# Performance work log

Measured on AMD Instinct MI355X. Metric: run time of the kernel, lower is better.

Reference implementation:

```python
import jax, jax.numpy as jnp
import numpy as np

B, N, DIM, H, DH, M = 4, 1024, 1024, 16, 64, 16  # batch, seq, model dim, heads, head dim, num_mem_kv
QK_SCALE = 10.0  # qk_norm_scale


def l2norm(t, eps=1e-12):
    # F.normalize(t, dim=-1) with clamp_min(eps), groups=1
    n = jnp.linalg.norm(t, axis=-1, keepdims=True)
    return t / jnp.maximum(n, eps)


def rotate_half(x):
    # interleaved pairs: (x0,x1) -> (-x1, x0)
    x = x.reshape(*x.shape[:-1], -1, 2)
    x1, x2 = x[..., 0], x[..., 1]
    return jnp.stack((-x2, x1), axis=-1).reshape(*x.shape[:-2], x.shape[-2] * 2)


def apply_rope(t, freqs):
    # freqs: [n, d], t: [b, h, n, d]
    return t * jnp.cos(freqs) + rotate_half(t) * jnp.sin(freqs)


def setup_inputs() -> dict:
    key = jax.random.key(0)
    ks = jax.random.split(key, 14)
    x = jax.random.normal(ks[0], (B, N, DIM), dtype=jnp.float32)
    # rotary freqs: outer(pos, inv_freq) with each freq repeated twice (interleaved pairs)
    pos = jnp.arange(N, dtype=jnp.float32)
    inv_freq = 1.0 / (10000.0 ** (jnp.arange(0, DH, 2, dtype=jnp.float32) / DH))
    freqs = jnp.repeat(pos[:, None] * inv_freq[None, :], 2, axis=-1)  # [N, DH]
    s = 0.02
    Wq = jax.random.normal(ks[1], (DIM, H * DH), dtype=jnp.float32) * s
    Wk = jax.random.normal(ks[2], (DIM, H * DH), dtype=jnp.float32) * s
    Wv = jax.random.normal(ks[3], (DIM, H * DH), dtype=jnp.float32) * s
    q_scale = 1.0 + 0.1 * jax.random.normal(ks[4], (H, 1, DH), dtype=jnp.float32)
    k_scale = 1.0 + 0.1 * jax.random.normal(ks[5], (H, 1, DH), dtype=jnp.float32)
    mem_k = jax.random.normal(ks[6], (H, M, DH), dtype=jnp.float32)
    mem_v = jax.random.normal(ks[7], (H, M, DH), dtype=jnp.float32)
    W_pre = jnp.eye(H, dtype=jnp.float32) + 0.05 * jax.random.normal(ks[8], (H, H), dtype=jnp.float32)
    W_post = jnp.eye(H, dtype=jnp.float32) + 0.05 * jax.random.normal(ks[9], (H, H), dtype=jnp.float32)
    W_hgate = jax.random.normal(ks[10], (DIM, H), dtype=jnp.float32) * s
    b_hgate = jnp.full((H,), 2.0, dtype=jnp.float32)
    W_vgate = jax.random.normal(ks[11], (DIM, H * DH), dtype=jnp.float32) * s
    b_vgate = jnp.full((H * DH,), 2.0, dtype=jnp.float32)
    Wo = jax.random.normal(ks[12], (H * DH, DIM), dtype=jnp.float32) * s
    return dict(x=x, freqs=freqs, Wq=Wq, Wk=Wk, Wv=Wv, q_scale=q_scale, k_scale=k_scale,
                mem_k=mem_k, mem_v=mem_v, W_pre=W_pre, W_post=W_post,
                W_hgate=W_hgate, b_hgate=b_hgate, W_vgate=W_vgate, b_vgate=b_vgate, Wo=Wo)


def reference(x, freqs, Wq, Wk, Wv, q_scale, k_scale, mem_k, mem_v,
              W_pre, W_post, W_hgate, b_hgate, W_vgate, b_vgate, Wo):
    b, n, _ = x.shape
    # projections -> [b, h, n, dh]
    q = (x @ Wq).reshape(b, n, H, DH).transpose(0, 2, 1, 3)
    k = (x @ Wk).reshape(b, n, H, DH).transpose(0, 2, 1, 3)
    v = (x @ Wv).reshape(b, n, H, DH).transpose(0, 2, 1, 3)
    # qk l2-norm (groups=1) + learned per-head dim scales
    q = l2norm(q) * q_scale
    k = l2norm(k) * k_scale
    # rotary (xpos_scale = None -> scale 1)
    q = apply_rope(q, freqs)
    k = apply_rope(k, freqs)
    # memory key/values, prepended along the kv sequence axis
    mk = (l2norm(mem_k) * k_scale)[None].repeat(b, axis=0)  # [b,h,M,dh]
    mv = mem_v[None].repeat(b, axis=0)
    k = jnp.concatenate((mk, k), axis=-2)  # [b,h,M+n,dh]
    v = jnp.concatenate((mv, v), axis=-2)
    i, j = q.shape[-2], k.shape[-2]
    dots = jnp.einsum('bhid,bhjd->bhij', q, k) * QK_SCALE
    dots = jnp.einsum('bhij,gh->bgij', dots, W_pre)  # pre-softmax talking heads
    # causal mask (memory slots at the front are always visible)
    qpos = jnp.arange(i)
    kpos = jnp.arange(j)
    causal = kpos[None, :] > (qpos[:, None] + (j - i))  # True -> masked
    mask_value = -jnp.finfo(dots.dtype).max
    dots = jnp.where(causal[None, None], mask_value, dots)
    attn = jax.nn.softmax(dots, axis=-1)
    attn = jnp.einsum('bhij,gh->bgij', attn, W_post)  # post-softmax talking heads
    out = jnp.einsum('bhij,bhjd->bhid', attn, v)  # [b,h,n,dh]
    # per-head value gate
    head_gate = jax.nn.sigmoid(x @ W_hgate + b_hgate)  # [b,n,h]
    out = out * head_gate.transpose(0, 2, 1)[..., None]
    out = out.transpose(0, 2, 1, 3).reshape(b, n, H * DH)
    # per-dim value gate (sigmoid)
    out = out * jax.nn.sigmoid(x @ W_vgate + b_vgate)
    return out @ Wo
```

## Files before the change

### kernel.cpp

```cpp
#include <hip/hip_runtime.h>
#include <hip/hip_bf16.h>
#include <cmath>

typedef __attribute__((ext_vector_type(8))) short short8;
typedef __attribute__((ext_vector_type(4))) float f32x4;

__device__ __forceinline__ unsigned short to_bf(float f) {
  __hip_bfloat16 h = __float2bfloat16(f);
  return __builtin_bit_cast(unsigned short, h);
}

__global__ __launch_bounds__(256)
void cvt_bf16x4(const float* __restrict__ in, unsigned short* __restrict__ out, int n4)
{
  int i = blockIdx.x * 256 + threadIdx.x;
  if (i < n4) {
    float4 v = ((const float4*)in)[i];
    ushort4 o;
    o.x = to_bf(v.x); o.y = to_bf(v.y); o.z = to_bf(v.z); o.w = to_bf(v.w);
    ((ushort4*)out)[i] = o;
  }
}

__global__ __launch_bounds__(256)
void transpose_to_bf(const float* __restrict__ W, unsigned short* __restrict__ WT)
{
  __shared__ float tile[64][65];
  const int n0 = blockIdx.x * 64, k0 = blockIdx.y * 64;
  const int t = threadIdx.x, c = t & 63, r4 = t >> 6;
#pragma unroll
  for (int q = 0; q < 16; ++q) {
    int r = (q << 2) + r4;
    tile[r][c] = W[(size_t)(k0 + r) * 1024 + n0 + c];
  }
  __syncthreads();
#pragma unroll
  for (int q = 0; q < 16; ++q) {
    int r = (q << 2) + r4;
    WT[(size_t)(n0 + r) * 1024 + k0 + c] = to_bf(tile[c][r]);
  }
}

__global__ __launch_bounds__(256)
void gemm_bf128(const unsigned short* __restrict__ A, const unsigned short* __restrict__ BT,
                float* __restrict__ C, unsigned short* __restrict__ Vout,
                const float* __restrict__ bias2, int mode)
{
  __shared__ __align__(16) unsigned short Ab[128 * 40];
  __shared__ __align__(16) unsigned short Bb[128 * 40];
  const int t = threadIdx.x, lane = t & 63, w = t >> 6;
  const int m = lane & 15, quad = lane >> 4;
  const int wm = w & 1, wn = w >> 1;
  const int row0 = blockIdx.y << 7, col0 = blockIdx.x << 7;

  const int c0 = t,        r0 = c0 >> 2, kp0 = c0 & 3;
  const int c1 = t + 256,  r1 = c1 >> 2, kp1 = c1 & 3;

  f32x4 acc[4][4];
#pragma unroll
  for (int mi = 0; mi < 4; ++mi)
#pragma unroll
    for (int ni = 0; ni < 4; ++ni) acc[mi][ni] = (f32x4){0.f, 0.f, 0.f, 0.f};

  uint4 pa0 = *(const uint4*)(A + (size_t)(row0 + r0) * 1024 + kp0 * 8);
  uint4 pa1 = *(const uint4*)(A + (size_t)(row0 + r1) * 1024 + kp1 * 8);
  uint4 pb0 = *(const uint4*)(BT + (size_t)(col0 + r0) * 1024 + kp0 * 8);
  uint4 pb1 = *(const uint4*)(BT + (size_t)(col0 + r1) * 1024 + kp1 * 8);

  for (int kk = 0; kk < 1024; kk += 32) {
    *(uint4*)((char*)Ab + r0 * 80 + kp0 * 16) = pa0;
    *(uint4*)((char*)Ab + r1 * 80 + kp1 * 16) = pa1;
    *(uint4*)((char*)Bb + r0 * 80 + kp0 * 16) = pb0;
    *(uint4*)((char*)Bb + r1 * 80 + kp1 * 16) = pb1;
    __syncthreads();
    if (kk + 32 < 1024) {
      pa0 = *(const uint4*)(A + (size_t)(row0 + r0) * 1024 + kk + 32 + kp0 * 8);
      pa1 = *(const uint4*)(A + (size_t)(row0 + r1) * 1024 + kk + 32 + kp1 * 8);
      pb0 = *(const uint4*)(BT + (size_t)(col0 + r0) * 1024 + kk + 32 + kp0 * 8);
      pb1 = *(const uint4*)(BT + (size_t)(col0 + r1) * 1024 + kk + 32 + kp1 * 8);
    }
    short8 af[4], bf[4];
#pragma unroll
    for (int mi = 0; mi < 4; ++mi)
      af[mi] = *(const short8*)((char*)Ab + ((wm << 6) + (mi << 4) + m) * 80 + quad * 16);
#pragma unroll
    for (int ni = 0; ni < 4; ++ni)
      bf[ni] = *(const short8*)((char*)Bb + ((wn << 6) + (ni << 4) + m) * 80 + quad * 16);
#pragma unroll
    for (int mi = 0; mi < 4; ++mi)
#pragma unroll
      for (int ni = 0; ni < 4; ++ni)
        acc[mi][ni] = __builtin_amdgcn_mfma_f32_16x16x32_bf16(af[mi], bf[ni], acc[mi][ni], 0, 0, 0);
    __syncthreads();
  }
#pragma unroll
  for (int mi = 0; mi < 4; ++mi)
#pragma unroll
    for (int ni = 0; ni < 4; ++ni)
#pragma unroll
      for (int reg = 0; reg < 4; ++reg) {
        int mrow = row0 + (wm << 6) + (mi << 4) + (quad << 2) + reg;
        int ncol = col0 + (wn << 6) + (ni << 4) + m;
        float v = acc[mi][ni][reg];
        if (mode == 0) {
          C[((size_t)mrow << 10) + ncol] = v;
        } else if (mode == 2) {
          float s = v + bias2[ncol];
          C[((size_t)mrow << 10) + ncol] = 1.f / (1.f + __expf(-s));
        } else {
          int bb = mrow >> 10, nn = mrow & 1023;
          Vout[((size_t)((bb << 10) + ncol)) * 1056 + 16 + nn] = to_bf(v);
        }
      }
}

__global__ __launch_bounds__(256)
void hgate_proj(const float* __restrict__ x, const float* __restrict__ W,
                const float* __restrict__ bias, float* __restrict__ hg)
{
  int G = blockIdx.x * 256 + threadIdx.x;
  int row = G >> 4, h = G & 15;
  const float4* x4 = (const float4*)(x + ((size_t)row << 10));
  float acc = 0.f;
#pragma unroll 4
  for (int k4 = 0; k4 < 256; ++k4) {
    float4 xv = x4[k4];
    int kb = k4 << 2;
    acc += xv.x * W[(kb + 0) * 16 + h] + xv.y * W[(kb + 1) * 16 + h]
         + xv.z * W[(kb + 2) * 16 + h] + xv.w * W[(kb + 3) * 16 + h];
  }
  float v = acc + bias[h];
  hg[(row << 4) + h] = 1.f / (1.f + __expf(-v));
}

__global__ __launch_bounds__(256)
void q_post_bf(const float* __restrict__ q_lin, const float* __restrict__ scale,
               const float* __restrict__ freqs, unsigned short* __restrict__ qb)
{
  int gid = blockIdx.x * 256 + threadIdx.x;
  int d = gid & 63;
  int row = gid >> 6;
  int h = row & 15;
  int n = (row >> 4) & 1023;
  float v = q_lin[gid];
  float ss = v * v;
#pragma unroll
  for (int off = 32; off; off >>= 1) ss += __shfl_xor(ss, off);
  v = v / fmaxf(sqrtf(ss), 1e-12f) * scale[(h << 6) + d];
  float f = freqs[(n << 6) + d];
  float other = __shfl_xor(v, 1);
  float rot = (d & 1) ? other : -other;
  qb[gid] = to_bf((v * cosf(f) + rot * sinf(f)) * 10.f);
}

__global__ __launch_bounds__(256)
void k_post_bf(const float* __restrict__ k_lin, const float* __restrict__ scale,
               const float* __restrict__ freqs, unsigned short* __restrict__ kall)
{
  int gid = blockIdx.x * 256 + threadIdx.x;
  int d = gid & 63;
  int row = gid >> 6;
  int h = row & 15;
  int n = (row >> 4) & 1023;
  int b = row >> 14;
  float v = k_lin[gid];
  float ss = v * v;
#pragma unroll
  for (int off = 32; off; off >>= 1) ss += __shfl_xor(ss, off);
  v = v / fmaxf(sqrtf(ss), 1e-12f) * scale[(h << 6) + d];
  float f = freqs[(n << 6) + d];
  float other = __shfl_xor(v, 1);
  float rot = (d & 1) ? other : -other;
  float out = v * cosf(f) + rot * sinf(f);
  kall[(size_t)(b * 1056 + 16 + n) * 1024 + (h << 6) + d] = to_bf(out);
}

__global__ __launch_bounds__(256)
void mem_build(const float* __restrict__ mem_k, const float* __restrict__ mem_v,
               const float* __restrict__ k_scale,
               unsigned short* __restrict__ kall, unsigned short* __restrict__ vallT)
{
  int gid = blockIdx.x * 256 + threadIdx.x;
  int d = gid & 63;
  int row = gid >> 6;
  int h = row >> 4, mm = row & 15;
  float v = mem_k[gid];
  float ss = v * v;
#pragma unroll
  for (int off = 32; off; off >>= 1) ss += __shfl_xor(ss, off);
  unsigned short kb = to_bf(v / fmaxf(sqrtf(ss), 1e-12f) * k_scale[(h << 6) + d]);
  unsigned short vb = to_bf(mem_v[gid]);
#pragma unroll
  for (int b = 0; b < 4; ++b) {
    kall[(size_t)(b * 1056 + mm) * 1024 + (h << 6) + d] = kb;
    vallT[(size_t)((b << 10) + (h << 6) + d) * 1056 + mm] = vb;
  }
}


__global__ __launch_bounds__(256, 3)
void attn_lsum(const unsigned short* __restrict__ qb, const unsigned short* __restrict__ kall,
               const float* __restrict__ W_pre, float* __restrict__ Lbuf)
{
  __shared__ float sS[16 * 16 * 33];
  __shared__ f32x4 sWpre4[64];

  const int t = threadIdx.x, lane = t & 63, w = t >> 6;
  const int m = lane & 15, quad = lane >> 4;
  if (t < 64) {
    int h = t >> 2, p4 = t & 3;
    sWpre4[t] = (f32x4){W_pre[(4 * p4 + 0) * 16 + h], W_pre[(4 * p4 + 1) * 16 + h],
                        W_pre[(4 * p4 + 2) * 16 + h], W_pre[(4 * p4 + 3) * 16 + h]};
  }

  const int blk = blockIdx.x;
  const int u0 = (4352 * blk) >> 10, u1 = (4352 * (blk + 1)) >> 10;
  if (u0 == u1) return;

  int accu = 0, bi = 0;
  while (true) {
    int un = (((bi & 63) + 1) >> 1) + 1;
    if (accu + un > u0) break;
    accu += un; ++bi;
  }
  int b = bi >> 6, it = bi & 63, uoff = u0 - accu;

  short8 afr[4][2];
  float partL[16];
  bool fresh = true;

  for (int u = u0; u < u1; ++u) {
    const int i0 = it << 4;
    if (fresh) {
#pragma unroll
      for (int hh = 0; hh < 4; ++hh)
#pragma unroll
        for (int kk = 0; kk < 2; ++kk)
          afr[hh][kk] = *(const short8*)(qb + (((size_t)(b << 10) + i0 + m) << 10)
                                         + ((w << 2) + hh) * 64 + kk * 32 + quad * 8);
#pragma unroll
      for (int g = 0; g < 16; ++g) partL[g] = 0.f;
      fresh = false;
    }
    const int j0 = uoff << 5;
#pragma unroll
    for (int sub = 0; sub < 2; ++sub) {
      const int js = j0 + (sub << 4);
#pragma unroll
      for (int hh = 0; hh < 4; ++hh) {
        f32x4 s = (f32x4){0.f, 0.f, 0.f, 0.f};
#pragma unroll
        for (int kk = 0; kk < 2; ++kk) {
          short8 bfr = *(const short8*)(kall + ((size_t)(b * 1056 + js + m) << 10)
                                        + ((w << 2) + hh) * 64 + kk * 32 + quad * 8);
          s = __builtin_amdgcn_mfma_f32_16x16x32_bf16(afr[hh][kk], bfr, s, 0, 0, 0);
        }
#pragma unroll
        for (int reg = 0; reg < 4; ++reg)
          sS[(((w << 2) + hh) * 16 + (quad << 2) + reg) * 33 + (sub << 4) + m] = s[reg];
      }
    }
    __syncthreads();
    {
      const int i_l = t >> 4, j_l = t & 15;
      const int ig = i0 + i_l;
      float ch0[16], ch1[16];
#pragma unroll
      for (int h = 0; h < 16; ++h) {
        ch0[h] = sS[(h * 16 + i_l) * 33 + j_l];
        ch1[h] = sS[(h * 16 + i_l) * 33 + 16 + j_l];
      }
      f32x4 a0[4], a1[4];
#pragma unroll
      for (int p = 0; p < 4; ++p) { a0[p] = (f32x4){0.f,0.f,0.f,0.f}; a1[p] = a0[p]; }
#pragma unroll
      for (int h = 0; h < 16; ++h) {
        float c0 = ch0[h], c1 = ch1[h];
#pragma unroll
        for (int p = 0; p < 4; ++p) {
          f32x4 wv = sWpre4[(h << 2) + p];
          a0[p] += wv * c0;
          a1[p] += wv * c1;
        }
      }
      const bool ok0 = (j0 + j_l) <= ig + 16;
      const bool ok1 = (j0 + 16 + j_l) <= ig + 16;
#pragma unroll
      for (int p = 0; p < 4; ++p)
#pragma unroll
        for (int e = 0; e < 4; ++e) {
          float v0 = ok0 ? __expf(a0[p][e] - 20.f) : 0.f;
          float v1 = ok1 ? __expf(a1[p][e] - 20.f) : 0.f;
          partL[(p << 2) + e] += v0 + v1;
        }
    }
    __syncthreads();
    ++uoff;
    if (uoff == ((it + 1) >> 1) + 1) {
#pragma unroll
      for (int g = 0; g < 16; ++g) {
        float v = partL[g];
        v += __shfl_xor(v, 1); v += __shfl_xor(v, 2);
        v += __shfl_xor(v, 4); v += __shfl_xor(v, 8);
        if (m == 0)
          atomicAdd(&Lbuf[(((size_t)(b << 10) + i0 + (w << 2) + quad) << 4) + g], v);
      }
      ++bi; b = bi >> 6; it = bi & 63; uoff = 0; fresh = true;
    }
  }
  if (!fresh) {
    const int i0 = it << 4;
#pragma unroll
    for (int g = 0; g < 16; ++g) {
      float v = partL[g];
      v += __shfl_xor(v, 1); v += __shfl_xor(v, 2);
      v += __shfl_xor(v, 4); v += __shfl_xor(v, 8);
      if (m == 0)
        atomicAdd(&Lbuf[(((size_t)(b << 10) + i0 + (w << 2) + quad) << 4) + g], v);
    }
  }
}

__global__ __launch_bounds__(256)
void attn_pv2(const unsigned short* __restrict__ qb, const unsigned short* __restrict__ kall,
              const unsigned short* __restrict__ vallT, const float* __restrict__ W_pre,
              const float* __restrict__ W_post, const float* __restrict__ Lbuf,
              float* __restrict__ Obuf)
{
  __shared__ float sS[16 * 16 * 33];
  __shared__ unsigned short sE[16 * 16 * 40];
  __shared__ f32x4 sWpre4[64], sWpost4[64];
  __shared__ float sIL[256];

  const int t = threadIdx.x, lane = t & 63, w = t >> 6;
  const int m = lane & 15, quad = lane >> 4;
  if (t < 64) {
    int h = t >> 2, p4 = t & 3;
    sWpre4[t]  = (f32x4){W_pre[(4 * p4 + 0) * 16 + h],  W_pre[(4 * p4 + 1) * 16 + h],
                         W_pre[(4 * p4 + 2) * 16 + h],  W_pre[(4 * p4 + 3) * 16 + h]};
    sWpost4[t] = (f32x4){W_post[(4 * p4 + 0) * 16 + h], W_post[(4 * p4 + 1) * 16 + h],
                         W_post[(4 * p4 + 2) * 16 + h], W_post[(4 * p4 + 3) * 16 + h]};
  }

  const int blk = blockIdx.x;
  const int u0 = (4352 * blk) >> 9, u1 = (4352 * (blk + 1)) >> 9;
  if (u0 == u1) return;

  int accu = 0, bi = 0;
  while (true) {
    int un = (((bi & 63) + 1) >> 1) + 1;
    if (accu + un > u0) break;
    accu += un; ++bi;
  }
  int b = bi >> 6, it = bi & 63, uoff = u0 - accu;

  short8 afr[4][2];
  f32x4 oacc[4][4];
  bool fresh = true;

  for (int u = u0; u < u1; ++u) {
    const int i0 = it << 4;
    if (fresh) {
#pragma unroll
      for (int hh = 0; hh < 4; ++hh)
#pragma unroll
        for (int kk = 0; kk < 2; ++kk)
          afr[hh][kk] = *(const short8*)(qb + (((size_t)(b << 10) + i0 + m) << 10)
                                         + ((w << 2) + hh) * 64 + kk * 32 + quad * 8);
#pragma unroll
      for (int a = 0; a < 4; ++a)
#pragma unroll
        for (int dt = 0; dt < 4; ++dt) oacc[a][dt] = (f32x4){0.f, 0.f, 0.f, 0.f};
      sIL[t] = 1.f / Lbuf[(((size_t)(b << 10) + i0 + (t >> 4)) << 4) + (t & 15)];
      fresh = false;
    }
    const int j0 = uoff << 5;
#pragma unroll
    for (int sub = 0; sub < 2; ++sub) {
      const int js = j0 + (sub << 4);
#pragma unroll
      for (int hh = 0; hh < 4; ++hh) {
        f32x4 s = (f32x4){0.f, 0.f, 0.f, 0.f};
#pragma unroll
        for (int kk = 0; kk < 2; ++kk) {
          short8 bfr = *(const short8*)(kall + ((size_t)(b * 1056 + js + m) << 10)
                                        + ((w << 2) + hh) * 64 + kk * 32 + quad * 8);
          s = __builtin_amdgcn_mfma_f32_16x16x32_bf16(afr[hh][kk], bfr, s, 0, 0, 0);
        }
#pragma unroll
        for (int reg = 0; reg < 4; ++reg)
          sS[(((w << 2) + hh) * 16 + (quad << 2) + reg) * 33 + (sub << 4) + m] = s[reg];
      }
    }
    __syncthreads();
    {
      const int i_l = t >> 4, j_l = t & 15;
      const int ig = i0 + i_l;
      float ch0[16], ch1[16];
#pragma unroll
      for (int h = 0; h < 16; ++h) {
        ch0[h] = sS[(h * 16 + i_l) * 33 + j_l];
        ch1[h] = sS[(h * 16 + i_l) * 33 + 16 + j_l];
      }
      f32x4 a0[4], a1[4];
#pragma unroll
      for (int p = 0; p < 4; ++p) { a0[p] = (f32x4){0.f,0.f,0.f,0.f}; a1[p] = a0[p]; }
#pragma unroll
      for (int h = 0; h < 16; ++h) {
        float c0 = ch0[h], c1 = ch1[h];
#pragma unroll
        for (int p = 0; p < 4; ++p) {
          f32x4 wv = sWpre4[(h << 2) + p];
          a0[p] += wv * c0;
          a1[p] += wv * c1;
        }
      }
      const bool ok0 = (j0 + j_l) <= ig + 16;
      const bool ok1 = (j0 + 16 + j_l) <= ig + 16;
      float e0[16], e1[16];
#pragma unroll
      for (int p = 0; p < 4; ++p)
#pragma unroll
        for (int e = 0; e < 4; ++e) {
          int g = (p << 2) + e;
          float il = sIL[(i_l << 4) + g];
          e0[g] = ok0 ? __expf(a0[p][e] - 20.f) * il : 0.f;
          e1[g] = ok1 ? __expf(a1[p][e] - 20.f) * il : 0.f;
        }
      f32x4 b0[4], b1[4];
#pragma unroll
      for (int p = 0; p < 4; ++p) { b0[p] = (f32x4){0.f,0.f,0.f,0.f}; b1[p] = b0[p]; }
#pragma unroll
      for (int g = 0; g < 16; ++g) {
        float c0 = e0[g], c1 = e1[g];
#pragma unroll
        for (int p = 0; p < 4; ++p) {
          f32x4 wv = sWpost4[(g << 2) + p];
          b0[p] += wv * c0;
          b1[p] += wv * c1;
        }
      }
#pragma unroll
      for (int p = 0; p < 4; ++p)
#pragma unroll
        for (int e = 0; e < 4; ++e) {
          int g2 = (p << 2) + e;
          sE[(g2 * 16 + i_l) * 40 + j_l] = to_bf(b0[p][e]);
          sE[(g2 * 16 + i_l) * 40 + 16 + j_l] = to_bf(b1[p][e]);
        }
    }
    __syncthreads();
#pragma unroll
    for (int gl = 0; gl < 4; ++gl) {
      const int g2 = (w << 2) + gl;
      short8 a = *(const short8*)((const char*)sE + ((g2 * 16 + m) * 40 + quad * 8) * 2);
#pragma unroll
      for (int dt = 0; dt < 4; ++dt) {
        short8 bv = *(const short8*)(vallT + ((size_t)((b << 10) + g2 * 64 + dt * 16 + m)) * 1056
                                     + j0 + quad * 8);
        oacc[gl][dt] = __builtin_amdgcn_mfma_f32_16x16x32_bf16(a, bv, oacc[gl][dt], 0, 0, 0);
      }
    }
    ++uoff;
    if (uoff == ((it + 1) >> 1) + 1) {
#pragma unroll
      for (int gl = 0; gl < 4; ++gl) {
        int g2 = (w << 2) + gl;
#pragma unroll
        for (int dt = 0; dt < 4; ++dt)
#pragma unroll
          for (int reg = 0; reg < 4; ++reg)
            atomicAdd(&Obuf[(((size_t)(b << 10) + i0 + (quad << 2) + reg) << 10)
                            + g2 * 64 + dt * 16 + m], oacc[gl][dt][reg]);
      }
      ++bi; b = bi >> 6; it = bi & 63; uoff = 0; fresh = true;
    }
  }
  if (!fresh) {
    const int i0 = it << 4;
#pragma unroll
    for (int gl = 0; gl < 4; ++gl) {
      int g2 = (w << 2) + gl;
#pragma unroll
      for (int dt = 0; dt < 4; ++dt)
#pragma unroll
        for (int reg = 0; reg < 4; ++reg)
          atomicAdd(&Obuf[(((size_t)(b << 10) + i0 + (quad << 2) + reg) << 10)
                          + g2 * 64 + dt * 16 + m], oacc[gl][dt][reg]);
    }
  }
}

__global__ __launch_bounds__(256)
void gate_out(const float* __restrict__ Obuf, const float* __restrict__ hgate,
              const float* __restrict__ vgate, unsigned short* __restrict__ aob)
{
  int i4 = blockIdx.x * 256 + threadIdx.x;
  float4 o = ((const float4*)Obuf)[i4];
  int base = i4 << 2;
  int row = base >> 10, hd = base & 1023, h = hd >> 6;
  float hg = hgate[(row << 4) + h];
  float4 vg = ((const float4*)vgate)[i4];
  ushort4 r;
  r.x = to_bf(o.x * hg * vg.x);
  r.y = to_bf(o.y * hg * vg.y);
  r.z = to_bf(o.z * hg * vg.z);
  r.w = to_bf(o.w * hg * vg.w);
  ((ushort4*)aob)[i4] = r;
}

extern "C" void kernel_launch(void* const* d_in, const int* in_sizes, int n_in,
                              void* d_out, int out_size, void* d_ws, size_t ws_size,
                              hipStream_t stream)
{
  const float* x       = (const float*)d_in[0];
  const float* freqs   = (const float*)d_in[1];
  const float* Wq      = (const float*)d_in[2];
  const float* Wk      = (const float*)d_in[3];
  const float* Wv      = (const float*)d_in[4];
  const float* q_scale = (const float*)d_in[5];
  const float* k_scale = (const float*)d_in[6];
  const float* mem_k   = (const float*)d_in[7];
  const float* mem_v   = (const float*)d_in[8];
  const float* W_pre   = (const float*)d_in[9];
  const float* W_post  = (const float*)d_in[10];
  const float* W_hg    = (const float*)d_in[11];
  const float* b_hg    = (const float*)d_in[12];
  const float* W_vg    = (const float*)d_in[13];
  const float* b_vg    = (const float*)d_in[14];
  const float* Wo      = (const float*)d_in[15];
  float* out = (float*)d_out;
  float* ws  = (float*)d_ws;

  float* q_lin = ws;
  unsigned short* aob = (unsigned short*)ws;
  float* Lbuf  = ws + 4128768;
  float* k_lin = ws + 4194304;
  float* Obuf  = k_lin;
  float* vgbuf = ws + 8388608;
  float* hgbuf = ws + 12582912;
  unsigned short* xb   = (unsigned short*)(ws + 12713984);
  unsigned short* qb   = xb;
  unsigned short* kall = (unsigned short*)(ws + 14811136);
  unsigned short* vallT= (unsigned short*)(ws + 16973824);
  unsigned short* wb   = (unsigned short*)(ws + 19136512);

  dim3 blk(256);
  cvt_bf16x4<<<4096, blk, 0, stream>>>(x, xb, 1048576);
  hgate_proj<<<256, blk, 0, stream>>>(x, W_hg, b_hg, hgbuf);
  transpose_to_bf<<<dim3(16, 16), blk, 0, stream>>>(Wq, wb);
  gemm_bf128<<<dim3(8, 32), blk, 0, stream>>>(xb, wb, q_lin, nullptr, nullptr, 0);
  transpose_to_bf<<<dim3(16, 16), blk, 0, stream>>>(Wk, wb);
  gemm_bf128<<<dim3(8, 32), blk, 0, stream>>>(xb, wb, k_lin, nullptr, nullptr, 0);
  transpose_to_bf<<<dim3(16, 16), blk, 0, stream>>>(Wv, wb);
  gemm_bf128<<<dim3(8, 32), blk, 0, stream>>>(xb, wb, nullptr, vallT, nullptr, 1);
  transpose_to_bf<<<dim3(16, 16), blk, 0, stream>>>(W_vg, wb);
  gemm_bf128<<<dim3(8, 32), blk, 0, stream>>>(xb, wb, vgbuf, nullptr, b_vg, 2);
  q_post_bf<<<16384, blk, 0, stream>>>(q_lin, q_scale, freqs, qb);
  k_post_bf<<<16384, blk, 0, stream>>>(k_lin, k_scale, freqs, kall);
  mem_build<<<64, blk, 0, stream>>>(mem_k, mem_v, k_scale, kall, vallT);
  hipMemsetAsync(Lbuf, 0, (65536 + 4194304) * sizeof(float), stream);
  attn_lsum<<<1024, blk, 0, stream>>>(qb, kall, W_pre, Lbuf);
  attn_pv2<<<512, blk, 0, stream>>>(qb, kall, vallT, W_pre, W_post, Lbuf, Obuf);
  gate_out<<<4096, blk, 0, stream>>>(Obuf, hgbuf, vgbuf, aob);
  transpose_to_bf<<<dim3(16, 16), blk, 0, stream>>>(Wo, wb);
  gemm_bf128<<<dim3(8, 32), blk, 0, stream>>>(aob, wb, out, nullptr, nullptr, 0);
}
```

Measured before the change: 558.4 us.

## Swizzle attention LDS tiles and rebalance attention grids to 768 blocks

```diff
diff --git a/kernel.cpp b/kernel.cpp
--- a/kernel.cpp
+++ b/kernel.cpp
@@ -9,6 +9,8 @@
   __hip_bfloat16 h = __float2bfloat16(f);
   return __builtin_bit_cast(unsigned short, h);
 }
+
+#define SWZS(ir) ((((ir) & 1) << 4) | (((ir) & 6) << 1))
 
 __global__ __launch_bounds__(256)
 void cvt_bf16x4(const float* __restrict__ in, unsigned short* __restrict__ out, int n4)
@@ -202,7 +204,7 @@
 void attn_lsum(const unsigned short* __restrict__ qb, const unsigned short* __restrict__ kall,
                const float* __restrict__ W_pre, float* __restrict__ Lbuf)
 {
-  __shared__ float sS[16 * 16 * 33];
+  __shared__ float sS[16 * 16 * 32];
   __shared__ f32x4 sWpre4[64];
 
   const int t = threadIdx.x, lane = t & 63, w = t >> 6;
@@ -214,7 +216,7 @@
   }
 
   const int blk = blockIdx.x;
-  const int u0 = (4352 * blk) >> 10, u1 = (4352 * (blk + 1)) >> 10;
+  const int u0 = (4352 * blk) / 768, u1 = (4352 * (blk + 1)) / 768;
   if (u0 == u1) return;
 
   int accu = 0, bi = 0;
@@ -256,19 +258,23 @@
           s = __builtin_amdgcn_mfma_f32_16x16x32_bf16(afr[hh][kk], bfr, s, 0, 0, 0);
         }
 #pragma unroll
-        for (int reg = 0; reg < 4; ++reg)
-          sS[(((w << 2) + hh) * 16 + (quad << 2) + reg) * 33 + (sub << 4) + m] = s[reg];
+        for (int reg = 0; reg < 4; ++reg) {
+          int irow = (quad << 2) + reg;
+          sS[(((w << 2) + hh) * 16 + irow) * 32 + (((sub << 4) + m) ^ SWZS(irow))] = s[reg];
+        }
       }
     }
     __syncthreads();
     {
       const int i_l = t >> 4, j_l = t & 15;
       const int ig = i0 + i_l;
+      const int vs = SWZS(i_l);
+      const int sc0 = j_l ^ vs, sc1 = (16 + j_l) ^ vs;
       float ch0[16], ch1[16];
 #pragma unroll
       for (int h = 0; h < 16; ++h) {
-        ch0[h] = sS[(h * 16 + i_l) * 33 + j_l];
-        ch1[h] = sS[(h * 16 + i_l) * 33 + 16 + j_l];
+        ch0[h] = sS[(h * 16 + i_l) * 32 + sc0];
+        ch1[h] = sS[(h * 16 + i_l) * 32 + sc1];
       }
       f32x4 a0[4], a1[4];
 #pragma unroll
@@ -321,14 +327,14 @@
   }
 }
 
-__global__ __launch_bounds__(256)
+__global__ __launch_bounds__(256, 3)
 void attn_pv2(const unsigned short* __restrict__ qb, const unsigned short* __restrict__ kall,
               const unsigned short* __restrict__ vallT, const float* __restrict__ W_pre,
               const float* __restrict__ W_post, const float* __restrict__ Lbuf,
               float* __restrict__ Obuf)
 {
-  __shared__ float sS[16 * 16 * 33];
-  __shared__ unsigned short sE[16 * 16 * 40];
+  __shared__ float sS[16 * 16 * 32];
+  __shared__ __align__(16) unsigned short sE[16 * 16 * 32];
   __shared__ f32x4 sWpre4[64], sWpost4[64];
   __shared__ float sIL[256];
 
@@ -343,7 +349,7 @@
   }
 
   const int blk = blockIdx.x;
-  const int u0 = (4352 * blk) >> 9, u1 = (4352 * (blk + 1)) >> 9;
+  const int u0 = (4352 * blk) / 768, u1 = (4352 * (blk + 1)) / 768;
   if (u0 == u1) return;
 
   int accu = 0, bi = 0;
@@ -388,19 +394,26 @@
           s = __builtin_amdgcn_mfma_f32_16x16x32_bf16(afr[hh][kk], bfr, s, 0, 0, 0);
         }
 #pragma unroll
-        for (int reg = 0; reg < 4; ++reg)
-          sS[(((w << 2) + hh) * 16 + (quad << 2) + reg) * 33 + (sub << 4) + m] = s[reg];
+        for (int reg = 0; reg < 4; ++reg) {
+          int irow = (quad << 2) + reg;
+          sS[(((w << 2) + hh) * 16 + irow) * 32 + (((sub << 4) + m) ^ SWZS(irow))] = s[reg];
+        }
       }
     }
     __syncthreads();
     {
       const int i_l = t >> 4, j_l = t & 15;
       const int ig = i0 + i_l;
+      const int vs = SWZS(i_l);
+      const int sc0 = j_l ^ vs, sc1 = (16 + j_l) ^ vs;
+      const int r3s = i_l & 3;
+      const int eo0 = ((((j_l >> 3) ^ r3s) << 3) | (j_l & 7));
+      const int eo1 = ((((2 + (j_l >> 3)) ^ r3s) << 3) | (j_l & 7));
       float ch0[16], ch1[16];
 #pragma unroll
       for (int h = 0; h < 16; ++h) {
-        ch0[h] = sS[(h * 16 + i_l) * 33 + j_l];
-        ch1[h] = sS[(h * 16 + i_l) * 33 + 16 + j_l];
+        ch0[h] = sS[(h * 16 + i_l) * 32 + sc0];
+        ch1[h] = sS[(h * 16 + i_l) * 32 + sc1];
       }
       f32x4 a0[4], a1[4];
 #pragma unroll
@@ -445,15 +458,15 @@
 #pragma unroll
         for (int e = 0; e < 4; ++e) {
           int g2 = (p << 2) + e;
-          sE[(g2 * 16 + i_l) * 40 + j_l] = to_bf(b0[p][e]);
-          sE[(g2 * 16 + i_l) * 40 + 16 + j_l] = to_bf(b1[p][e]);
+          sE[(g2 * 16 + i_l) * 32 + eo0] = to_bf(b0[p][e]);
+          sE[(g2 * 16 + i_l) * 32 + eo1] = to_bf(b1[p][e]);
         }
     }
     __syncthreads();
 #pragma unroll
     for (int gl = 0; gl < 4; ++gl) {
       const int g2 = (w << 2) + gl;
-      short8 a = *(const short8*)((const char*)sE + ((g2 * 16 + m) * 40 + quad * 8) * 2);
+      short8 a = *(const short8*)(sE + (g2 * 16 + m) * 32 + ((quad ^ (m & 3)) << 3));
 #pragma unroll
       for (int dt = 0; dt < 4; ++dt) {
         short8 bv = *(const short8*)(vallT + ((size_t)((b << 10) + g2 * 64 + dt * 16 + m)) * 1056
@@ -560,8 +573,8 @@
   k_post_bf<<<16384, blk, 0, stream>>>(k_lin, k_scale, freqs, kall);
   mem_build<<<64, blk, 0, stream>>>(mem_k, mem_v, k_scale, kall, vallT);
   hipMemsetAsync(Lbuf, 0, (65536 + 4194304) * sizeof(float), stream);
-  attn_lsum<<<1024, blk, 0, stream>>>(qb, kall, W_pre, Lbuf);
-  attn_pv2<<<512, blk, 0, stream>>>(qb, kall, vallT, W_pre, W_post, Lbuf, Obuf);
+  attn_lsum<<<768, blk, 0, stream>>>(qb, kall, W_pre, Lbuf);
+  attn_pv2<<<768, blk, 0, stream>>>(qb, kall, vallT, W_pre, W_post, Lbuf, Obuf);
   gate_out<<<4096, blk, 0, stream>>>(Obuf, hgbuf, vgbuf, aob);
   transpose_to_bf<<<dim3(16, 16), blk, 0, stream>>>(Wo, wb);
   gemm_bf128<<<dim3(8, 32), blk, 0, stream>>>(aob, wb, out, nullptr, nullptr, 0);
```

New measurement: 594.6 us. +6.5%, slower.
